# Kernel optimization log

Measured on AMD Instinct MI355X. Metric: run time of the kernel, lower is better.

Reference implementation:

```python
import jax, jax.numpy as jnp
import numpy as np

N_NODES = 10000
N_EDGES = 320000
AVG_NEIGH = 32.0


def ssp(x):
    # ShiftedSoftPlus
    return jax.nn.softplus(x) - jnp.asarray(np.log(2.0), x.dtype)


def setup_inputs() -> dict:
    key = jax.random.key(0)
    ks = jax.random.split(key, 16)
    inp = {
        "node_feats0": jax.random.normal(ks[0], (N_NODES, 64), jnp.float32),
        "node_feats1": jax.random.normal(ks[1], (N_NODES, 64, 3), jnp.float32),
        "node_attrs": jax.random.uniform(ks[2], (N_NODES, 4), jnp.float32),
        "edge_embedding": jax.random.uniform(ks[3], (N_EDGES, 8), jnp.float32),
        "edge_attrs": jax.random.normal(ks[4], (N_EDGES, 4), jnp.float32),
        "edge_src": jax.random.randint(ks[5], (N_EDGES,), 0, N_NODES),
        "edge_dst": jax.random.randint(ks[6], (N_EDGES,), 0, N_NODES),
        "W1_0": jax.random.normal(ks[7], (64, 64), jnp.float32),
        "W1_1": jax.random.normal(ks[8], (64, 64), jnp.float32),
        "Wr1": jax.random.normal(ks[9], (8, 8), jnp.float32),
        "Wr2": jax.random.normal(ks[10], (8, 256), jnp.float32),
        "W2_0": jax.random.normal(ks[11], (128, 128), jnp.float32),
        "W2_1": jax.random.normal(ks[12], (128, 64), jnp.float32),
        "Wsc_0": jax.random.normal(ks[13], (64, 4, 128), jnp.float32),
        "Wsc_1": jax.random.normal(ks[14], (64, 4, 64), jnp.float32),
    }
    return inp


def _tfn_layer(node_feats0, node_feats1, node_attrs, edge_embedding, edge_attrs,
               edge_src, edge_dst, W1_0, W1_1, Wr1, Wr2, W2_0, W2_1, Wsc_0, Wsc_1):
    N = node_feats0.shape[0]
    # --- linear_1 (e3nn Linear: per-irrep block, 1/sqrt(fan_in)) ---
    x0 = (node_feats0 @ W1_0) / jnp.sqrt(64.0)                       # [N,64]
    x1 = jnp.einsum('nuc,uw->nwc', node_feats1, W1_1) / jnp.sqrt(64.0)  # [N,64,3]
    # --- radial MLP: 8 -> 8 (ssp) -> 256, no bias ---
    h = ssp(edge_embedding @ Wr1 / jnp.sqrt(8.0))
    w = (h @ Wr2 / jnp.sqrt(8.0)).reshape(-1, 4, 64)                  # [E,4,64]
    # --- gather source node features ---
    xs0 = x0[edge_src]                                                # [E,64]
    xs1 = x1[edge_src]                                                # [E,64,3]
    y0 = edge_attrs[:, 0:1]                                           # [E,1] (0e SH)
    y1 = edge_attrs[:, 1:4]                                           # [E,3] (1o SH)
    # --- per-edge equivariant tensor product (uvu, 4 instructions) ---
    m00 = w[:, 0] * xs0 * y0                                          # 0e x 0e -> 0e
    m01 = w[:, 1][:, :, None] * xs0[:, :, None] * y1[:, None, :]      # 0e x 1o -> 1o
    m10 = w[:, 2][:, :, None] * xs1 * y0[:, :, None]                  # 1o x 0e -> 1o
    m11 = w[:, 3] * jnp.einsum('euc,ec->eu', xs1, y1) / jnp.sqrt(3.0)  # 1o x 1o -> 0e
    mid0 = jnp.concatenate([m00, m11], axis=1)                        # [E,128]
    mid1 = jnp.concatenate([m01, m10], axis=1)                        # [E,128,3]
    # --- scatter-sum to destination nodes, / sqrt(avg_num_neighbors) ---
    agg0 = jax.ops.segment_sum(mid0, edge_dst, num_segments=N) / jnp.sqrt(AVG_NEIGH)
    agg1 = jax.ops.segment_sum(mid1, edge_dst, num_segments=N) / jnp.sqrt(AVG_NEIGH)
    # --- linear_2 to conv output irreps 128x0e + 64x1o ---
    out0 = (agg0 @ W2_0) / jnp.sqrt(128.0)                            # [N,128]
    out1 = jnp.einsum('nuc,uw->nwc', agg1, W2_1) / jnp.sqrt(128.0)    # [N,64,3]
    # --- self connection: FullyConnectedTensorProduct(node_feats_in, node_attrs) ---
    sc0 = jnp.einsum('nu,nv,uvw->nw', node_feats0, node_attrs, Wsc_0) / jnp.sqrt(256.0)
    sc1 = jnp.einsum('nuc,nv,uvw->nwc', node_feats1, node_attrs, Wsc_1) / jnp.sqrt(256.0)
    n0 = out0 + sc0
    n1 = out1 + sc1
    # --- Gate nonlinearity: 64 scalars (ssp), 64 gates (ssp) gating 64x1o ---
    scalars = ssp(n0[:, :64])
    gates = ssp(n0[:, 64:])
    gated = n1 * gates[:, :, None]
    # --- resnet ---
    new0 = node_feats0 + scalars
    new1 = node_feats1 + gated
    return jnp.concatenate([new0, new1.reshape(N, 192)], axis=1)      # [N,256]


def reference(node_feats0, node_feats1, node_attrs, edge_embedding, edge_attrs,
              edge_src, edge_dst, W1_0, W1_1, Wr1, Wr2, W2_0, W2_1, Wsc_0, Wsc_1):
    return _tfn_layer(node_feats0, node_feats1, node_attrs, edge_embedding, edge_attrs,
                      edge_src, edge_dst, W1_0, W1_1, Wr1, Wr2, W2_0, W2_1, Wsc_0, Wsc_1)
```

## Files before the change

### kernel.cpp

```cpp
#include <hip/hip_runtime.h>
#include <math.h>

#define N_NODES 10000
#define N_EDGES 320000
#define DEG_CAP 96

typedef short bf16x8 __attribute__((ext_vector_type(8)));
typedef float f32x4 __attribute__((ext_vector_type(4)));

__device__ __forceinline__ float ssp(float x) {
    float ax = fabsf(x);
    return fmaxf(x, 0.0f) + log1pf(expf(-ax)) - 0.69314718055994531f;
}
__device__ __forceinline__ float bcastf(float v, int l) {
    return __uint_as_float(__builtin_amdgcn_readlane(__float_as_uint(v), l));
}
__device__ __forceinline__ int bcasti(int v, int l) {
    return __builtin_amdgcn_readlane(v, l);
}
__device__ __forceinline__ int div3(int q) {
    return (q * 21846) >> 16;
}
__device__ __forceinline__ unsigned short f2bf(float f) {
    unsigned int u = __float_as_uint(f);
    u += 0x7fff + ((u >> 16) & 1);
    return (unsigned short)(u >> 16);
}


__global__ __launch_bounds__(256) void wprep_kernel(
    const float* __restrict__ W2_0, const float* __restrict__ Wsc0,
    const float* __restrict__ W2_1, const float* __restrict__ Wsc1,
    uint4* __restrict__ wb0, uint4* __restrict__ wb1)
{
    const int tid = blockIdx.x*256 + threadIdx.x;
    const float rs128 = 0.088388347648318447f;
    const float s16 = 0.0625f;
    if (tid < 6144) {
        const int kstep = tid >> 9;
        const int rem = tid & 511;
        const int col = ((rem >> 6) << 4) + (rem & 15);
        const int kb = kstep*32 + (((rem & 63) >> 4) << 3);
        unsigned int u[4];
        #pragma unroll
        for (int h = 0; h < 4; ++h) {
            const int k0 = kb + 2*h, k1 = k0 + 1;
            const float f0 = (k0 < 128) ? W2_0[k0*128+col]*rs128 : Wsc0[(k0-128)*128+col]*s16;
            const float f1 = (k1 < 128) ? W2_0[k1*128+col]*rs128 : Wsc0[(k1-128)*128+col]*s16;
            u[h] = (unsigned int)f2bf(f0) | ((unsigned int)f2bf(f1) << 16);
        }
        wb0[tid] = make_uint4(u[0], u[1], u[2], u[3]);
    } else if (tid < 9216) {
        const int t2 = tid - 6144;
        const int kstep = t2 >> 8;
        const int rem = t2 & 255;
        const int col = ((rem >> 6) << 4) + (rem & 15);
        const int kb = kstep*32 + (((rem & 63) >> 4) << 3);
        unsigned int u[4];
        #pragma unroll
        for (int h = 0; h < 4; ++h) {
            const int k0 = kb + 2*h, k1 = k0 + 1;
            const float f0 = (k0 < 128) ? W2_1[k0*64+col]*rs128 : Wsc1[(k0-128)*64+col]*s16;
            const float f1 = (k1 < 128) ? W2_1[k1*64+col]*rs128 : Wsc1[(k1-128)*64+col]*s16;
            u[h] = (unsigned int)f2bf(f0) | ((unsigned int)f2bf(f1) << 16);
        }
        wb1[t2] = make_uint4(u[0], u[1], u[2], u[3]);
    }
}


__global__ __launch_bounds__(256) void node_pre_kernel(
        const float* __restrict__ nf0, const float* __restrict__ nf1,
        const float* __restrict__ W1_0, const float* __restrict__ W1_1,
        const int* __restrict__ edst, const int* __restrict__ esrc,
        int* __restrict__ counts, int2* __restrict__ csr2,
        uint2* __restrict__ xpack) {
    const int n = blockIdx.x;
    const int t = threadIdx.x;
    __shared__ float s_f0[64];
    __shared__ float s_f1[192];
    __shared__ unsigned short sx[4][64];
    if (t < 64) s_f0[t] = nf0[n*64 + t];
    else        s_f1[t-64] = nf1[n*192 + (t-64)];
    if (t >= 224) {
        int e = n*32 + (t - 224);
        int d = edst[e];
        int sv = esrc[e];
        int p = atomicAdd(&counts[d], 1);
        if (p < DEG_CAP) csr2[d * DEG_CAP + p] = make_int2(e, sv);
    }
    __syncthreads();
    if (t < 64) {
        float acc = 0.f;
        #pragma unroll 8
        for (int u = 0; u < 64; ++u) acc += s_f0[u] * W1_0[u*64 + t];
        sx[0][t] = f2bf(acc * 0.125f);
    } else {
        const int c = (t - 64) >> 6;
        const int w = t & 63;
        float acc = 0.f;
        #pragma unroll 8
        for (int u = 0; u < 64; ++u) acc += s_f1[u*3 + c] * W1_1[u*64 + w];
        sx[1+c][w] = f2bf(acc * 0.125f);
    }
    __syncthreads();
    if (t < 64) {
        uint2 v;
        v.x = (unsigned int)sx[0][t] | ((unsigned int)sx[1][t] << 16);
        v.y = (unsigned int)sx[2][t] | ((unsigned int)sx[3][t] << 16);
        xpack[(size_t)n*64 + t] = v;
    }
}


__global__ __launch_bounds__(256) void edge_kernel(
    const float* __restrict__ eemb, const float* __restrict__ eattr,
    const int* __restrict__ counts, const int2* __restrict__ csr2,
    const uint2* __restrict__ xpack,
    const float* __restrict__ Wr1, const float* __restrict__ Wr2,
    unsigned int* __restrict__ agg0p, unsigned int* __restrict__ agg1p)
{
    const int wid = threadIdx.x >> 6;
    const int nl  = wid >> 1;
    const int p   = wid & 1;
    const int n   = blockIdx.x * 2 + nl;
    const int u   = threadIdx.x & 63;
    const int j8  = u & 7;

    const float rs8 = 0.35355339059327373f;
    const float rs3 = 0.57735026918962576f;

    float wr2[4][8];
    #pragma unroll
    for (int k = 0; k < 4; ++k) {
        #pragma unroll
        for (int j = 0; j < 8; ++j) {
            float v = Wr2[j*256 + k*64 + u] * rs8;
            wr2[k][j] = (k == 3) ? v * rs3 : v;
        }
    }
    float wr1c[8];
    #pragma unroll
    for (int i = 0; i < 8; ++i) wr1c[i] = Wr1[i*8 + j8] * rs8;

    float A[8] = {0.f,0.f,0.f,0.f,0.f,0.f,0.f,0.f};

    const int craw = counts[n];
    const int cnt  = craw < DEG_CAP ? craw : DEG_CAP;
    const int base0 = n * DEG_CAP;

    int2 es = make_int2(0, 0);
    float4 m0 = {0,0,0,0}, m1 = {0,0,0,0};
    float yy = 0.f;
    uint2 g[8];
    #pragma unroll
    for (int s = 0; s < 8; ++s) g[s] = make_uint2(0u, 0u);

    const int b0 = p*8;
    if (b0 < cnt) {
        const int mm = cnt - b0 < 8 ? cnt - b0 : 8;
        const int sl = (u >> 3) < mm ? (u >> 3) : 0;
        es = csr2[base0 + b0 + sl];
        m0 = *reinterpret_cast<const float4*>(eemb + (size_t)es.x*8);
        m1 = *reinterpret_cast<const float4*>(eemb + (size_t)es.x*8 + 4);
        yy = eattr[(size_t)es.x*4 + (j8 & 3)];
        #pragma unroll
        for (int s = 0; s < 8; ++s)
            g[s] = xpack[(size_t)bcasti(es.y, s*8)*64 + u];
    }

    for (int b = b0; b < cnt; b += 16) {
        const int m = cnt - b < 8 ? cnt - b : 8;
        const float4 cm0 = m0, cm1 = m1;
        const float cy = yy;
        uint2 cg[8];
        #pragma unroll
        for (int s = 0; s < 8; ++s) cg[s] = g[s];

        const int bn = b + 16;
        const bool more = (bn < cnt);
        int2 esn = make_int2(0, 0);
        if (more) {
            const int mn = cnt - bn < 8 ? cnt - bn : 8;
            const int sn = (u >> 3) < mn ? (u >> 3) : 0;
            esn = csr2[base0 + bn + sn];
        }

        float pre = cm0.x*wr1c[0] + cm0.y*wr1c[1] + cm0.z*wr1c[2] + cm0.w*wr1c[3]
                  + cm1.x*wr1c[4] + cm1.y*wr1c[5] + cm1.z*wr1c[6] + cm1.w*wr1c[7];
        const float h = ssp(pre);

        if (more) {
            es = esn;
            m0 = *reinterpret_cast<const float4*>(eemb + (size_t)es.x*8);
            m1 = *reinterpret_cast<const float4*>(eemb + (size_t)es.x*8 + 4);
            yy = eattr[(size_t)es.x*4 + (j8 & 3)];
            #pragma unroll
            for (int s = 0; s < 8; ++s)
                g[s] = xpack[(size_t)bcasti(es.y, s*8)*64 + u];
        }

        #pragma unroll
        for (int s = 0; s < 8; ++s) {
            if (s >= m) break;
            const int bs = s * 8;
            const float xs0 = __uint_as_float(cg[s].x << 16);
            const float x1a = __uint_as_float(cg[s].x & 0xffff0000u);
            const float x1b = __uint_as_float(cg[s].y << 16);
            const float x1c = __uint_as_float(cg[s].y & 0xffff0000u);
            float w0 = 0.f, w1 = 0.f, w2 = 0.f, w3 = 0.f;
            #pragma unroll
            for (int j = 0; j < 8; ++j) {
                const float hj = bcastf(h, bs + j);
                w0 += hj * wr2[0][j];
                w1 += hj * wr2[1][j];
                w2 += hj * wr2[2][j];
                w3 += hj * wr2[3][j];
            }
            const float y0 = bcastf(cy, bs+0);
            const float y1 = bcastf(cy, bs+1);
            const float y2 = bcastf(cy, bs+2);
            const float y3 = bcastf(cy, bs+3);
            A[0] += w0 * xs0 * y0;
            const float t01 = w1 * xs0;
            A[1] += t01*y1; A[2] += t01*y2; A[3] += t01*y3;
            const float t10 = w2 * y0;
            A[4] += t10*x1a; A[5] += t10*x1b; A[6] += t10*x1c;
            A[7] += w3 * (x1a*y1 + x1b*y2 + x1c*y3);
        }
    }

    __shared__ float red[2][2][8][64];
    #pragma unroll
    for (int a = 0; a < 8; ++a) red[nl][p][a][u] = A[a];
    __syncthreads();

    const float rs32 = 0.17677669529663687f;
    if (threadIdx.x < 128) {
        const int nlq = threadIdx.x >> 6;
        const int kp  = threadIdx.x & 63;
        const int a   = (kp < 32) ? 0 : 7;
        const int uu0 = (kp < 32) ? 2*kp : 2*kp - 64;
        const float v0 = (red[nlq][0][a][uu0]   + red[nlq][1][a][uu0])   * rs32;
        const float v1 = (red[nlq][0][a][uu0+1] + red[nlq][1][a][uu0+1]) * rs32;
        const int nn = blockIdx.x*2 + nlq;
        agg0p[(size_t)nn*64 + kp] = (unsigned int)f2bf(v0) | ((unsigned int)f2bf(v1) << 16);
    }
    #pragma unroll
    for (int it = 0; it < 2; ++it) {
        const int idx = it*256 + threadIdx.x;
        if (idx < 384) {
            const int nlq = (idx >= 192) ? 1 : 0;
            const int pi  = idx - nlq*192;
            const int c   = pi >> 6, kp = pi & 63;
            const int a   = (kp < 32) ? (1+c) : (4+c);
            const int u0  = (kp < 32) ? (2*kp) : (2*kp - 64);
            const float v0 = (red[nlq][0][a][u0]   + red[nlq][1][a][u0])   * rs32;
            const float v1 = (red[nlq][0][a][u0+1] + red[nlq][1][a][u0+1]) * rs32;
            const int nn = blockIdx.x*2 + nlq;
            agg1p[(size_t)nn*192 + pi] = (unsigned int)f2bf(v0) | ((unsigned int)f2bf(v1) << 16);
        }
    }
}


__global__ __launch_bounds__(512) void epiA_mfma_kernel(
    const float* __restrict__ nf0, const float* __restrict__ nattr,
    const unsigned int* __restrict__ agg0p, const uint4* __restrict__ wb0,
    float* __restrict__ out, float* __restrict__ gbuf)
{
    __shared__ unsigned int sA[3072];
    const int t = threadIdx.x;
    const int node0 = blockIdx.x * 16;

    #pragma unroll
    for (int it = 0; it < 6; ++it) {
        int idx = it*512 + t;
        int q = idx >> 6;
        int row = div3(q);
        int seg = q - 3*row;
        int kp = seg*64 + (idx & 63);
        int node = node0 + row;
        unsigned int val;
        if (kp < 64) val = agg0p[(size_t)node*64 + kp];
        else {
            int pk = kp - 64;
            float f = nf0[(size_t)node*64 + (pk >> 1)];
            const float2 at = *reinterpret_cast<const float2*>(nattr + (size_t)node*4 + ((pk & 1) << 1));
            val = (unsigned int)f2bf(f*at.x) | ((unsigned int)f2bf(f*at.y) << 16);
        }
        sA[row*192 + (kp ^ ((row & 7) << 2))] = val;
    }
    __syncthreads();

    const int ct = t >> 6;
    const int lane = t & 63;
    const int m = lane & 15;
    const int ks = lane >> 4;
    const char* sab = reinterpret_cast<const char*>(sA) + m*768;
    const int swz = (m & 7) << 4;

    f32x4 acc = {0.f, 0.f, 0.f, 0.f};
    #pragma unroll
    for (int kstep = 0; kstep < 12; ++kstep) {
        bf16x8 a = *reinterpret_cast<const bf16x8*>(sab + (((kstep << 6) + (ks << 4)) ^ swz));
        bf16x8 b = *reinterpret_cast<const bf16x8*>(wb0 + (kstep << 9) + (ct << 6) + lane);
        acc = __builtin_amdgcn_mfma_f32_16x16x32_bf16(a, b, acc, 0, 0, 0);
    }

    const int col = ct*16 + m;
    #pragma unroll
    for (int q = 0; q < 4; ++q) {
        const int node = node0 + ks*4 + q;
        const float v = ssp(acc[q]);
        if (col < 64) out[(size_t)node*256 + col] = nf0[(size_t)node*64 + col] + v;
        else          gbuf[(size_t)node*64 + (col - 64)] = v;
    }
}


__global__ __launch_bounds__(256) void epiB_mfma_kernel(
    const float* __restrict__ nf1, const float* __restrict__ nattr,
    const unsigned int* __restrict__ agg1p, const uint4* __restrict__ wb1,
    const float* __restrict__ gbuf, float* __restrict__ out)
{
    __shared__ unsigned int sB[3072];
    const int t = threadIdx.x;
    const int row0 = blockIdx.x * 16;

    #pragma unroll
    for (int it = 0; it < 12; ++it) {
        int idx = it*256 + t;
        int q = idx >> 6;
        int row = div3(q);
        int seg = q - 3*row;
        int kp = seg*64 + (idx & 63);
        int r = row0 + row;
        int n = div3(r);
        int c = r - 3*n;
        unsigned int val;
        if (kp < 64) val = agg1p[(size_t)n*192 + c*64 + kp];
        else {
            int pk = kp - 64;
            float f = nf1[(size_t)n*192 + (pk >> 1)*3 + c];
            const float2 at = *reinterpret_cast<const float2*>(nattr + (size_t)n*4 + ((pk & 1) << 1));
            val = (unsigned int)f2bf(f*at.x) | ((unsigned int)f2bf(f*at.y) << 16);
        }
        sB[row*192 + (kp ^ ((row & 7) << 2))] = val;
    }
    __syncthreads();

    const int ct = t >> 6;
    const int lane = t & 63;
    const int m = lane & 15;
    const int ks = lane >> 4;
    const char* sab = reinterpret_cast<const char*>(sB) + m*768;
    const int swz = (m & 7) << 4;

    f32x4 acc = {0.f, 0.f, 0.f, 0.f};
    #pragma unroll
    for (int kstep = 0; kstep < 12; ++kstep) {
        bf16x8 a = *reinterpret_cast<const bf16x8*>(sab + (((kstep << 6) + (ks << 4)) ^ swz));
        bf16x8 b = *reinterpret_cast<const bf16x8*>(wb1 + (kstep << 8) + (ct << 6) + lane);
        acc = __builtin_amdgcn_mfma_f32_16x16x32_bf16(a, b, acc, 0, 0, 0);
    }

    const int col = ct*16 + m;
    #pragma unroll
    for (int q = 0; q < 4; ++q) {
        const int r = row0 + ks*4 + q;
        const int n = div3(r);
        const int c = r - 3*n;
        const float g = gbuf[(size_t)n*64 + col];
        out[(size_t)n*256 + 64 + col*3 + c] = nf1[(size_t)n*192 + col*3 + c] + acc[q]*g;
    }
}


extern "C" void kernel_launch(void* const* d_in, const int* in_sizes, int n_in,
                              void* d_out, int out_size, void* d_ws, size_t ws_size,
                              hipStream_t stream) {
    const float* nf0   = (const float*)d_in[0];
    const float* nf1   = (const float*)d_in[1];
    const float* nattr = (const float*)d_in[2];
    const float* eemb  = (const float*)d_in[3];
    const float* eattr = (const float*)d_in[4];
    const int*   esrc  = (const int*)d_in[5];
    const int*   edst  = (const int*)d_in[6];
    const float* W1_0  = (const float*)d_in[7];
    const float* W1_1  = (const float*)d_in[8];
    const float* Wr1   = (const float*)d_in[9];
    const float* Wr2   = (const float*)d_in[10];
    const float* W2_0  = (const float*)d_in[11];
    const float* W2_1  = (const float*)d_in[12];
    const float* Wsc0  = (const float*)d_in[13];
    const float* Wsc1  = (const float*)d_in[14];
    float* out = (float*)d_out;

    char* ws = (char*)d_ws;
    uint2* xpack = (uint2*)ws;         ws += (size_t)N_NODES*64*sizeof(uint2);
    int* counts  = (int*)ws;           ws += (size_t)N_NODES*sizeof(int);
    int2* csr2   = (int2*)ws;          ws += (size_t)N_NODES*DEG_CAP*sizeof(int2);
    unsigned int* agg0p = (unsigned int*)ws;
                                       ws += (size_t)N_NODES*64*sizeof(unsigned int);
    unsigned int* agg1p = (unsigned int*)ws;
                                       ws += (size_t)N_NODES*192*sizeof(unsigned int);
    uint4* wb0   = (uint4*)ws;         ws += (size_t)6144*sizeof(uint4);
    uint4* wb1   = (uint4*)ws;         ws += (size_t)3072*sizeof(uint4);
    float* gbuf  = (float*)csr2;

    hipMemsetAsync(counts, 0, N_NODES*sizeof(int), stream);
    wprep_kernel<<<36, 256, 0, stream>>>(W2_0, Wsc0, W2_1, Wsc1, wb0, wb1);
    node_pre_kernel<<<N_NODES, 256, 0, stream>>>(nf0, nf1, W1_0, W1_1, edst, esrc,
        counts, csr2, xpack);
    edge_kernel<<<(N_NODES+1)/2, 256, 0, stream>>>(eemb, eattr, counts, csr2,
        xpack, Wr1, Wr2, agg0p, agg1p);
    epiA_mfma_kernel<<<N_NODES/16, 512, 0, stream>>>(nf0, nattr, agg0p, wb0, out, gbuf);
    epiB_mfma_kernel<<<(3*N_NODES)/16, 256, 0, stream>>>(nf1, nattr, agg1p, wb1, gbuf, out);
}
```

Baseline: 130.7 us.

## Use one wavefront per node in edge kernel, drop LDS reduction

The edge kernel previously split each node's edges across two wavefronts (four waves per block, two nodes per block) and combined the partial sums through shared memory and a block barrier. Now each 64-thread block handles one node with a single wavefront walking all its edges in steps of 8. Lane pairs are packed to bf16 with a shuffle, and the writes go straight to global memory. This removes the LDS round-trip and the __syncthreads, but halves per-node parallelism, so high-degree nodes take longer serial loops and tail imbalance may grow.

```diff
diff --git a/kernel.cpp b/kernel.cpp
--- a/kernel.cpp
+++ b/kernel.cpp
@@ -113,19 +113,16 @@
 }
 
 
-__global__ __launch_bounds__(256) void edge_kernel(
+__global__ __launch_bounds__(64, 4) void edge_kernel(
     const float* __restrict__ eemb, const float* __restrict__ eattr,
     const int* __restrict__ counts, const int2* __restrict__ csr2,
     const uint2* __restrict__ xpack,
     const float* __restrict__ Wr1, const float* __restrict__ Wr2,
     unsigned int* __restrict__ agg0p, unsigned int* __restrict__ agg1p)
 {
-    const int wid = threadIdx.x >> 6;
-    const int nl  = wid >> 1;
-    const int p   = wid & 1;
-    const int n   = blockIdx.x * 2 + nl;
-    const int u   = threadIdx.x & 63;
-    const int j8  = u & 7;
+    const int n = blockIdx.x;
+    const int u = threadIdx.x;
+    const int j8 = u & 7;
 
     const float rs8 = 0.35355339059327373f;
     const float rs3 = 0.57735026918962576f;
@@ -156,11 +153,10 @@
     #pragma unroll
     for (int s = 0; s < 8; ++s) g[s] = make_uint2(0u, 0u);
 
-    const int b0 = p*8;
-    if (b0 < cnt) {
-        const int mm = cnt - b0 < 8 ? cnt - b0 : 8;
+    if (0 < cnt) {
+        const int mm = cnt < 8 ? cnt : 8;
         const int sl = (u >> 3) < mm ? (u >> 3) : 0;
-        es = csr2[base0 + b0 + sl];
+        es = csr2[base0 + sl];
         m0 = *reinterpret_cast<const float4*>(eemb + (size_t)es.x*8);
         m1 = *reinterpret_cast<const float4*>(eemb + (size_t)es.x*8 + 4);
         yy = eattr[(size_t)es.x*4 + (j8 & 3)];
@@ -169,7 +165,7 @@
             g[s] = xpack[(size_t)bcasti(es.y, s*8)*64 + u];
     }
 
-    for (int b = b0; b < cnt; b += 16) {
+    for (int b = 0; b < cnt; b += 8) {
         const int m = cnt - b < 8 ? cnt - b : 8;
         const float4 cm0 = m0, cm1 = m1;
         const float cy = yy;
@@ -177,7 +173,7 @@
         #pragma unroll
         for (int s = 0; s < 8; ++s) cg[s] = g[s];
 
-        const int bn = b + 16;
+        const int bn = b + 8;
         const bool more = (bn < cnt);
         int2 esn = make_int2(0, 0);
         if (more) {
@@ -230,35 +226,25 @@
         }
     }
 
-    __shared__ float red[2][2][8][64];
-    #pragma unroll
-    for (int a = 0; a < 8; ++a) red[nl][p][a][u] = A[a];
-    __syncthreads();
-
     const float rs32 = 0.17677669529663687f;
-    if (threadIdx.x < 128) {
-        const int nlq = threadIdx.x >> 6;
-        const int kp  = threadIdx.x & 63;
-        const int a   = (kp < 32) ? 0 : 7;
-        const int uu0 = (kp < 32) ? 2*kp : 2*kp - 64;
-        const float v0 = (red[nlq][0][a][uu0]   + red[nlq][1][a][uu0])   * rs32;
-        const float v1 = (red[nlq][0][a][uu0+1] + red[nlq][1][a][uu0+1]) * rs32;
-        const int nn = blockIdx.x*2 + nlq;
-        agg0p[(size_t)nn*64 + kp] = (unsigned int)f2bf(v0) | ((unsigned int)f2bf(v1) << 16);
-    }
-    #pragma unroll
-    for (int it = 0; it < 2; ++it) {
-        const int idx = it*256 + threadIdx.x;
-        if (idx < 384) {
-            const int nlq = (idx >= 192) ? 1 : 0;
-            const int pi  = idx - nlq*192;
-            const int c   = pi >> 6, kp = pi & 63;
-            const int a   = (kp < 32) ? (1+c) : (4+c);
-            const int u0  = (kp < 32) ? (2*kp) : (2*kp - 64);
-            const float v0 = (red[nlq][0][a][u0]   + red[nlq][1][a][u0])   * rs32;
-            const float v1 = (red[nlq][0][a][u0+1] + red[nlq][1][a][u0+1]) * rs32;
-            const int nn = blockIdx.x*2 + nlq;
-            agg1p[(size_t)nn*192 + pi] = (unsigned int)f2bf(v0) | ((unsigned int)f2bf(v1) << 16);
+    float v[8], pv[8];
+    #pragma unroll
+    for (int a = 0; a < 8; ++a) {
+        v[a] = A[a] * rs32;
+        pv[a] = __shfl_xor(v[a], 1);
+    }
+    if (!(u & 1)) {
+        const int kp = u >> 1;
+        unsigned int pk[8];
+        #pragma unroll
+        for (int a = 0; a < 8; ++a)
+            pk[a] = (unsigned int)f2bf(v[a]) | ((unsigned int)f2bf(pv[a]) << 16);
+        agg0p[(size_t)n*64 + kp]      = pk[0];
+        agg0p[(size_t)n*64 + 32 + kp] = pk[7];
+        #pragma unroll
+        for (int c = 0; c < 3; ++c) {
+            agg1p[(size_t)n*192 + c*64 + kp]      = pk[1+c];
+            agg1p[(size_t)n*192 + c*64 + 32 + kp] = pk[4+c];
         }
     }
 }
@@ -413,7 +399,7 @@
     wprep_kernel<<<36, 256, 0, stream>>>(W2_0, Wsc0, W2_1, Wsc1, wb0, wb1);
     node_pre_kernel<<<N_NODES, 256, 0, stream>>>(nf0, nf1, W1_0, W1_1, edst, esrc,
         counts, csr2, xpack);
-    edge_kernel<<<(N_NODES+1)/2, 256, 0, stream>>>(eemb, eattr, counts, csr2,
+    edge_kernel<<<N_NODES, 64, 0, stream>>>(eemb, eattr, counts, csr2,
         xpack, Wr1, Wr2, agg0p, agg1p);
     epiA_mfma_kernel<<<N_NODES/16, 512, 0, stream>>>(nf0, nattr, agg0p, wb0, out, gbuf);
     epiB_mfma_kernel<<<(3*N_NODES)/16, 256, 0, stream>>>(nf1, nattr, agg1p, wb1, gbuf, out);
```

After: 125.8 us. 1.04x faster.
